# Performance work log

Measured on AMD Instinct MI355X. Metric: run time of the kernel, lower is better.

## Reference

```python
import itertools
import jax, jax.numpy as jnp
import numpy as np

B = 1024      # graphs
N = 40        # atoms per graph (module supports 1..49)
ETA = 64
K = 32        # num_clusters
ZD = 32       # z_dim
NA = 10       # num_atom_types
NB = 5        # num_bond_types + 1
CH, AH, BH = 128, 128, 64
TAU = 1.0


def _resblock(x, W1, b1, W2, b2, Ws, bs):
    # assumed ResidualBlock: Linear->ReLU->(dropout, eval=identity)->Linear + linear skip
    h = jax.nn.relu(x @ W1 + b1)
    return h @ W2 + b2 + (x @ Ws + bs)


def setup_inputs() -> dict:
    key = jax.random.key(0)
    ks = jax.random.split(key, 24)
    s = 0.05
    pairs = np.array(list(itertools.combinations(range(N), 2)), dtype=np.int32)  # [780,2]
    offsets = (np.arange(B, dtype=np.int32) * N)[:, None, None]
    edge_index = jnp.asarray((pairs[None] + offsets).reshape(-1, 2))  # [B*780, 2]
    return {
        "eta": jax.random.normal(ks[0], (B, ETA), jnp.float32),
        "gumbel_noise": jax.random.gumbel(ks[1], (B * N, K), jnp.float32),
        "z_noise": jax.random.normal(ks[2], (B * N, ZD), jnp.float32),
        "cW1": jax.random.normal(ks[3], (ETA, CH)) * s, "cb1": jnp.zeros((CH,)),
        "cW2": jax.random.normal(ks[4], (CH, K)) * s, "cb2": jnp.zeros((K,)),
        "cWs": jax.random.normal(ks[5], (ETA, K)) * s, "cbs": jnp.zeros((K,)),
        "cluster_means": jax.random.normal(ks[6], (K, ZD)),
        "cluster_log_sigmas": jnp.full((K, ZD), -2.0),
        "aW1": jax.random.normal(ks[7], (ZD, AH)) * s, "ab1": jnp.zeros((AH,)),
        "aW2": jax.random.normal(ks[8], (AH, NA)) * s, "ab2": jnp.zeros((NA,)),
        "aWs": jax.random.normal(ks[9], (ZD, NA)) * s, "abs_": jnp.zeros((NA,)),
        "bond_matrix": jax.random.normal(ks[10], (NB, ZD, ZD)),
        "bW1": jax.random.normal(ks[11], (NB, BH)) * s, "bb1": jnp.zeros((BH,)),
        "bW2": jax.random.normal(ks[12], (BH, NB)) * s, "bb2": jnp.zeros((NB,)),
        "bWs": jax.random.normal(ks[13], (NB, NB)) * s, "bbs": jnp.zeros((NB,)),
        "edge_index": edge_index,
    }


def reference(eta, gumbel_noise, z_noise,
              cW1, cb1, cW2, cb2, cWs, cbs,
              cluster_means, cluster_log_sigmas,
              aW1, ab1, aW2, ab2, aWs, abs_,
              bond_matrix, bW1, bb1, bW2, bb2, bWs, bbs,
              edge_index):
    # decode_eta: mixture weights
    pi = jax.nn.softmax(_resblock(eta, cW1, cb1, cW2, cb2, cWs, cbs), axis=1)  # [B,K]
    log_pi = jnp.log(pi)
    # sample_c: gumbel-softmax (hard, straight-through) per node
    logits = jnp.repeat(log_pi, N, axis=0)                      # [B*N, K]
    y_soft = jax.nn.softmax((logits + gumbel_noise) / TAU, axis=-1)
    y_hard = jax.nn.one_hot(jnp.argmax(y_soft, axis=-1), K, dtype=y_soft.dtype)
    c = y_hard + y_soft - jax.lax.stop_gradient(y_soft)         # straight-through
    # sample_z
    mu = c @ cluster_means                                      # [B*N, ZD]
    log_sigma = c @ cluster_log_sigmas
    sigma = jnp.exp(jnp.clip(log_sigma, -20.0, 30.0))
    z = z_noise * sigma + mu
    # decode_z: atom logits
    atom_types = _resblock(z, aW1, ab1, aW2, ab2, aWs, abs_)    # [B*N, NA]
    # symmetrized per-bond-type bilinear form over edge node pairs
    Wsym = 0.5 * (bond_matrix + jnp.swapaxes(bond_matrix, 1, 2))  # [NB, ZD, ZD]
    zi = z[edge_index[:, 0]]                                    # [E, ZD]
    zj = z[edge_index[:, 1]]                                    # [E, ZD]
    bil = jnp.einsum('ed,tdc,ec->et', zi, Wsym, zj)             # [E, NB]
    edge_logits = _resblock(bil, bW1, bb1, bW2, bb2, bWs, bbs)
    edge_types = jax.nn.softmax(edge_logits, axis=1)            # [E, NB]
    return atom_types, edge_types
```

## Files before the change

kernel.cpp:

```cpp
#include <hip/hip_runtime.h>

constexpr int NPAIR = 780;

constexpr int OFF_ZT = 0;
constexpr int OFF_A  = 1280;
constexpr int UTP    = 1280;
constexpr int OFF_BT = 3840;
constexpr int SH_TOT = 7740;

typedef float v2f __attribute__((ext_vector_type(2)));
typedef float v4f __attribute__((ext_vector_type(4)));
union V4 { v4f v; v2f h[2]; float f[4]; };

__device__ __forceinline__ void pk_fma_lo(v2f& acc, v2f s2, v2f b) {
  asm("v_pk_fma_f32 %0, %1, %2, %0 op_sel:[0,0,0] op_sel_hi:[0,1,1]"
      : "+v"(acc) : "v"(s2), "v"(b));
}
__device__ __forceinline__ void pk_fma_hi(v2f& acc, v2f s2, v2f b) {
  asm("v_pk_fma_f32 %0, %1, %2, %0 op_sel:[1,0,0] op_sel_hi:[1,1,1]"
      : "+v"(acc) : "v"(s2), "v"(b));
}
__device__ __forceinline__ void pk_fma_vs(v2f& acc, v2f a, v2f b) {
  asm("v_pk_fma_f32 %0, %1, %2, %0 op_sel:[0,0,0] op_sel_hi:[1,1,1]"
      : "+v"(acc) : "v"(a), "s"(b));
}
__device__ __forceinline__ v2f pk_add(v2f a, v2f b) {
  v2f d; asm("v_pk_add_f32 %0, %1, %2" : "=v"(d) : "v"(a), "v"(b)); return d;
}
__device__ __forceinline__ v2f pk_addrelu(v2f a, v2f b) {
  v2f s = pk_add(a, b);
  v2f d; d.x = fmaxf(s.x, 0.f); d.y = fmaxf(s.y, 0.f);
  return d;
}

__global__ __launch_bounds__(256) void prep_kernel(
    const float* __restrict__ eta,
    const float* __restrict__ cW1, const float* __restrict__ cb1,
    const float* __restrict__ cW2, const float* __restrict__ cb2,
    const float* __restrict__ cWs, const float* __restrict__ cbs,
    const float* __restrict__ bond, const float* __restrict__ lsig,
    const float* __restrict__ bW1, const float* __restrict__ bb1,
    const float* __restrict__ bW2, const float* __restrict__ bb2,
    const float* __restrict__ bWs, const float* __restrict__ bbs,
    float* __restrict__ log_pi, float* __restrict__ wsym,
    float* __restrict__ sigma, float* __restrict__ hwg)
{
  if (blockIdx.x < 256) {
    const int lane = threadIdx.x & 63, wid = threadIdx.x >> 6;
    const int row = blockIdx.x * 4 + wid;
    __shared__ __align__(16) float etas[4][64];
    __shared__ __align__(16) float hs[4][128];
    etas[wid][lane] = eta[row * 64 + lane];
    __syncthreads();
    float a0 = cb1[lane], a1 = cb1[lane + 64];
    for (int d = 0; d < 64; ++d) {
      float ed = etas[wid][d];
      a0 += ed * cW1[d * 128 + lane];
      a1 += ed * cW1[d * 128 + lane + 64];
    }
    hs[wid][lane] = fmaxf(a0, 0.f);
    hs[wid][lane + 64] = fmaxf(a1, 0.f);
    __syncthreads();
    if (lane < 32) {
      float x = cb2[lane] + cbs[lane];
      for (int j = 0; j < 128; ++j) x += hs[wid][j] * cW2[j * 32 + lane];
      for (int d = 0; d < 64; ++d) x += etas[wid][d] * cWs[d * 32 + lane];
      float m = x;
      for (int off = 16; off; off >>= 1) m = fmaxf(m, __shfl_xor(m, off));
      float e = __expf(x - m);
      float s = e;
      for (int off = 16; off; off >>= 1) s += __shfl_xor(s, off);
      log_pi[row * 32 + lane] = (x - m) - __logf(s);
    }
  } else {
    const int e = (blockIdx.x - 256) * 256 + threadIdx.x;
    if (e < 5120) {
      const int t = e >> 10, r = e & 1023, c = r >> 5, d = r & 31;
      wsym[e] = 0.5f * (bond[e] + bond[t * 1024 + d * 32 + c]);
    } else if (e < 6144) {
      const int q = e - 5120;
      sigma[q] = __expf(fminf(fmaxf(lsig[q], -20.f), 30.f));
    } else if (e < 6888) {
      const int idx = e - 6144;
      float v;
      if (idx < 320) v = bW1[idx];
      else if (idx < 384) v = bb1[idx - 320];
      else if (idx < 704) { int qq = idx - 384; int t2 = qq >> 6, j = qq & 63; v = bW2[j * 5 + t2]; }
      else if (idx < 709) v = bb2[idx - 704];
      else if (idx < 734) v = bWs[idx - 709];
      else v = bbs[idx - 734];
      hwg[idx] = v;
    }
  }
}

__global__ __launch_bounds__(256, 5) void fused_kernel(
    const float* __restrict__ log_pi, const float* __restrict__ gumbel,
    const float* __restrict__ z_noise,
    const float* __restrict__ means, const float* __restrict__ sigma,
    const float* __restrict__ aW1, const float* __restrict__ ab1,
    const float* __restrict__ aW2, const float* __restrict__ ab2,
    const float* __restrict__ aWs, const float* __restrict__ abs_,
    const float* __restrict__ wsym, const float* __restrict__ hwg,
    float* __restrict__ atom_out, float* __restrict__ edge_out)
{
  __shared__ __align__(16) float S[SH_TOT];
  const int tid = threadIdx.x;
  const int lane = tid & 63, wid = tid >> 6;
  const int m = blockIdx.x;

  if (lane < 40) {
    const int n = wid * 10 + (lane >> 2);
    const int sub = lane & 3;
    const int c0 = sub * 8;
    const int n_glb = m * 40 + n;
    const float4* lp4 = (const float4*)(log_pi + m * 32 + c0);
    const float4* g4  = (const float4*)(gumbel + (size_t)n_glb * 32 + c0);
    const float4* zn4 = (const float4*)(z_noise + (size_t)n_glb * 32 + c0);
    float4 zn0 = zn4[0], zn1 = zn4[1];
    float vals[8];
    {
      float4 a = lp4[0], b = g4[0];
      vals[0] = a.x + b.x; vals[1] = a.y + b.y; vals[2] = a.z + b.z; vals[3] = a.w + b.w;
    }
    {
      float4 a = lp4[1], b = g4[1];
      vals[4] = a.x + b.x; vals[5] = a.y + b.y; vals[6] = a.z + b.z; vals[7] = a.w + b.w;
    }
    int kb = c0; float vb = vals[0];
    #pragma unroll
    for (int q = 1; q < 8; ++q)
      if (vals[q] > vb) { vb = vals[q]; kb = c0 + q; }
    #pragma unroll
    for (int off = 1; off <= 2; off <<= 1) {
      float vo = __shfl_xor(vb, off);
      int   ko = __shfl_xor(kb, off);
      if (vo > vb || (vo == vb && ko < kb)) { vb = vo; kb = ko; }
    }
    const float4* mk4 = (const float4*)(means + kb * 32 + c0);
    const float4* sg4 = (const float4*)(sigma + kb * 32 + c0);
    {
      float4 mk = mk4[0], sg = sg4[0];
      S[OFF_ZT + (c0    ) * 40 + n] = zn0.x * sg.x + mk.x;
      S[OFF_ZT + (c0 + 1) * 40 + n] = zn0.y * sg.y + mk.y;
      S[OFF_ZT + (c0 + 2) * 40 + n] = zn0.z * sg.z + mk.z;
      S[OFF_ZT + (c0 + 3) * 40 + n] = zn0.w * sg.w + mk.w;
    }
    {
      float4 mk = mk4[1], sg = sg4[1];
      S[OFF_ZT + (c0 + 4) * 40 + n] = zn1.x * sg.x + mk.x;
      S[OFF_ZT + (c0 + 5) * 40 + n] = zn1.y * sg.y + mk.y;
      S[OFF_ZT + (c0 + 6) * 40 + n] = zn1.z * sg.z + mk.z;
      S[OFF_ZT + (c0 + 7) * 40 + n] = zn1.w * sg.w + mk.w;
    }
  }
  __syncthreads();

  {
    for (int u = tid; u < 320; u += 256) {
      const int ng = u >> 5, jg = u & 31;
      const int n0 = ng * 4, j0 = jg * 4;
      v2f acc[4][2];
      #pragma unroll
      for (int a = 0; a < 4; ++a) { acc[a][0] = (v2f){0.f,0.f}; acc[a][1] = (v2f){0.f,0.f}; }
      #pragma unroll 8
      for (int c = 0; c < 32; ++c) {
        V4 zv; zv.v = *(const v4f*)&S[OFF_ZT + c * 40 + n0];
        V4 wv; wv.v = *(const v4f*)(aW1 + c * 128 + j0);
        pk_fma_lo(acc[0][0], zv.h[0], wv.h[0]); pk_fma_lo(acc[0][1], zv.h[0], wv.h[1]);
        pk_fma_hi(acc[1][0], zv.h[0], wv.h[0]); pk_fma_hi(acc[1][1], zv.h[0], wv.h[1]);
        pk_fma_lo(acc[2][0], zv.h[1], wv.h[0]); pk_fma_lo(acc[2][1], zv.h[1], wv.h[1]);
        pk_fma_hi(acc[3][0], zv.h[1], wv.h[0]); pk_fma_hi(acc[3][1], zv.h[1], wv.h[1]);
      }
      V4 bv; bv.v = *(const v4f*)(ab1 + j0);
      #pragma unroll
      for (int a = 0; a < 4; ++a) {
        V4 hv;
        hv.h[0] = pk_addrelu(acc[a][0], bv.h[0]);
        hv.h[1] = pk_addrelu(acc[a][1], bv.h[1]);
        *(v4f*)&S[OFF_A + (n0 + a) * 132 + j0] = hv.v;
      }
    }
  }
  __syncthreads();

  if (tid < 200) {
    const int n = tid / 5, kp = tid - (tid / 5) * 5, k0 = kp * 2;
    float a0 = ab2[k0] + abs_[k0];
    float a1 = ab2[k0 + 1] + abs_[k0 + 1];
    #pragma unroll 8
    for (int c = 0; c < 32; ++c) {
      float zc = S[OFF_ZT + c * 40 + n];
      float2 w = *(const float2*)(aWs + c * 10 + k0);
      a0 += zc * w.x; a1 += zc * w.y;
    }
    #pragma unroll 8
    for (int j = 0; j < 128; ++j) {
      float hv = S[OFF_A + n * 132 + j];
      float2 w = *(const float2*)(aW2 + j * 10 + k0);
      a0 += hv * w.x; a1 += hv * w.y;
    }
    *(float2*)(atom_out + (size_t)m * 400 + n * 10 + k0) = make_float2(a0, a1);
  }
  __syncthreads();

  #pragma unroll
  for (int R = 0; R < 3; ++R) {
    const int tbase = 2 * R;
    const int nplanes = (R == 2) ? 1 : 2;
    if (tid < nplanes * 80) {
      const int tl = tid / 80, r = tid - tl * 80;
      const int dg = r / 10, ig = r - dg * 10;
      const int d0 = dg * 4, i0 = ig * 4;
      const float* wg = wsym + (tbase + tl) * 1024;
      v2f acc[4][2];
      #pragma unroll
      for (int a = 0; a < 4; ++a) { acc[a][0] = (v2f){0.f,0.f}; acc[a][1] = (v2f){0.f,0.f}; }
      #pragma unroll 8
      for (int c = 0; c < 32; ++c) {
        V4 zv; zv.v = *(const v4f*)&S[OFF_ZT + c * 40 + i0];
        V4 wv; wv.v = *(const v4f*)(wg + c * 32 + d0);
        pk_fma_lo(acc[0][0], wv.h[0], zv.h[0]); pk_fma_lo(acc[0][1], wv.h[0], zv.h[1]);
        pk_fma_hi(acc[1][0], wv.h[0], zv.h[0]); pk_fma_hi(acc[1][1], wv.h[0], zv.h[1]);
        pk_fma_lo(acc[2][0], wv.h[1], zv.h[0]); pk_fma_lo(acc[2][1], wv.h[1], zv.h[1]);
        pk_fma_hi(acc[3][0], wv.h[1], zv.h[0]); pk_fma_hi(acc[3][1], wv.h[1], zv.h[1]);
      }
      #pragma unroll
      for (int a = 0; a < 4; ++a) {
        V4 st; st.h[0] = acc[a][0]; st.h[1] = acc[a][1];
        *(v4f*)&S[OFF_A + tl * UTP + (d0 + a) * 40 + i0] = st.v;
      }
    }
    __syncthreads();

    if (tid < nplanes * 55) {
      const int tl = tid / 55;
      int q = tid - tl * 55;
      int ig = 0;
      while (q >= 10 - ig) { q -= 10 - ig; ++ig; }
      const int jg = ig + q;
      const int i0 = ig * 4, j0 = jg * 4;
      v2f acc[4][2];
      #pragma unroll
      for (int a = 0; a < 4; ++a) { acc[a][0] = (v2f){0.f,0.f}; acc[a][1] = (v2f){0.f,0.f}; }
      #pragma unroll 8
      for (int d = 0; d < 32; ++d) {
        V4 uv; uv.v = *(const v4f*)&S[OFF_A + tl * UTP + d * 40 + i0];
        V4 zv; zv.v = *(const v4f*)&S[OFF_ZT + d * 40 + j0];
        pk_fma_lo(acc[0][0], uv.h[0], zv.h[0]); pk_fma_lo(acc[0][1], uv.h[0], zv.h[1]);
        pk_fma_hi(acc[1][0], uv.h[0], zv.h[0]); pk_fma_hi(acc[1][1], uv.h[0], zv.h[1]);
        pk_fma_lo(acc[2][0], uv.h[1], zv.h[0]); pk_fma_lo(acc[2][1], uv.h[1], zv.h[1]);
        pk_fma_hi(acc[3][0], uv.h[1], zv.h[0]); pk_fma_hi(acc[3][1], uv.h[1], zv.h[1]);
      }
      const int tg = tbase + tl;
      #pragma unroll
      for (int a = 0; a < 4; ++a) {
        const int i = i0 + a;
        V4 row; row.h[0] = acc[a][0]; row.h[1] = acc[a][1];
        #pragma unroll
        for (int b = 0; b < 4; ++b) {
          const int j = j0 + b;
          if (i < j) {
            const int p = i * (79 - i) / 2 + (j - i - 1);
            S[OFF_BT + tg * 780 + p] = row.f[b];
          }
        }
      }
    }
    __syncthreads();
  }

  const float* w1h = hwg;
  const float* b1h = hwg + 320;
  const float* w2t = hwg + 384;
  const float* b2h = hwg + 704;
  const float* wsh = hwg + 709;
  const float* bsh = hwg + 734;

  const bool htail = (tid < 12);
  float bil5[3][5];
  v2f bil2[3][5];
  v2f lg2[3][5];
  #pragma unroll
  for (int s = 0; s < 3; ++s) {
    const int p = tid + (s << 8);
    #pragma unroll
    for (int t = 0; t < 5; ++t) {
      float v = S[OFF_BT + t * 780 + p];
      bil5[s][t] = v;
      bil2[s][t].x = v; bil2[s][t].y = v;
    }
    #pragma unroll
    for (int t2 = 0; t2 < 5; ++t2) {
      float a = b2h[t2] + bsh[t2];
      #pragma unroll
      for (int t = 0; t < 5; ++t) a += bil5[s][t] * wsh[t * 5 + t2];
      lg2[s][t2].x = a; lg2[s][t2].y = 0.f;
    }
  }
  float bil3[5], lg3[5];
  if (htail) {
    const int p = 768 + tid;
    #pragma unroll
    for (int t = 0; t < 5; ++t) bil3[t] = S[OFF_BT + t * 780 + p];
    #pragma unroll
    for (int t2 = 0; t2 < 5; ++t2) {
      float a = b2h[t2] + bsh[t2];
      #pragma unroll
      for (int t = 0; t < 5; ++t) a += bil3[t] * wsh[t * 5 + t2];
      lg3[t2] = a;
    }
  }
  {
    for (int j4 = 0; j4 < 16; ++j4) {
      V4 bb; bb.v = *(const v4f*)(b1h + 4 * j4);
      v2f h2[3][2];
      #pragma unroll
      for (int s = 0; s < 3; ++s) { h2[s][0] = bb.h[0]; h2[s][1] = bb.h[1]; }
      #pragma unroll
      for (int t = 0; t < 5; ++t) {
        V4 w1; w1.v = *(const v4f*)(w1h + t * 64 + 4 * j4);
        #pragma unroll
        for (int s = 0; s < 3; ++s) {
          pk_fma_vs(h2[s][0], bil2[s][t], w1.h[0]);
          pk_fma_vs(h2[s][1], bil2[s][t], w1.h[1]);
        }
      }
      #pragma unroll
      for (int s = 0; s < 3; ++s) {
        h2[s][0].x = fmaxf(h2[s][0].x, 0.f); h2[s][0].y = fmaxf(h2[s][0].y, 0.f);
        h2[s][1].x = fmaxf(h2[s][1].x, 0.f); h2[s][1].y = fmaxf(h2[s][1].y, 0.f);
      }
      #pragma unroll
      for (int t2 = 0; t2 < 5; ++t2) {
        V4 w2; w2.v = *(const v4f*)(w2t + t2 * 64 + 4 * j4);
        #pragma unroll
        for (int s = 0; s < 3; ++s) {
          pk_fma_vs(lg2[s][t2], h2[s][0], w2.h[0]);
          pk_fma_vs(lg2[s][t2], h2[s][1], w2.h[1]);
        }
      }
      if (htail) {
        float4 h3 = make_float4(bb.f[0], bb.f[1], bb.f[2], bb.f[3]);
        #pragma unroll
        for (int t = 0; t < 5; ++t) {
          const float* w1p = w1h + t * 64 + 4 * j4;
          float bt = bil3[t];
          h3.x += bt * w1p[0]; h3.y += bt * w1p[1]; h3.z += bt * w1p[2]; h3.w += bt * w1p[3];
        }
        h3.x = fmaxf(h3.x, 0.f); h3.y = fmaxf(h3.y, 0.f);
        h3.z = fmaxf(h3.z, 0.f); h3.w = fmaxf(h3.w, 0.f);
        #pragma unroll
        for (int t2 = 0; t2 < 5; ++t2) {
          const float* w2p = w2t + t2 * 64 + 4 * j4;
          lg3[t2] += h3.x * w2p[0] + h3.y * w2p[1] + h3.z * w2p[2] + h3.w * w2p[3];
        }
      }
    }
  }
  #pragma unroll
  for (int s = 0; s < 3; ++s) {
    const int p = tid + (s << 8);
    float lgv[5];
    #pragma unroll
    for (int t2 = 0; t2 < 5; ++t2) lgv[t2] = lg2[s][t2].x + lg2[s][t2].y;
    float mx = lgv[0];
    #pragma unroll
    for (int t2 = 1; t2 < 5; ++t2) mx = fmaxf(mx, lgv[t2]);
    float e[5], sum = 0.f;
    #pragma unroll
    for (int t2 = 0; t2 < 5; ++t2) { e[t2] = __expf(lgv[t2] - mx); sum += e[t2]; }
    float inv = 1.f / sum;
    float* outp = edge_out + ((size_t)m * NPAIR + p) * 5;
    #pragma unroll
    for (int t2 = 0; t2 < 5; ++t2) outp[t2] = e[t2] * inv;
  }
  if (htail) {
    const int p = 768 + tid;
    float mx = lg3[0];
    #pragma unroll
    for (int t2 = 1; t2 < 5; ++t2) mx = fmaxf(mx, lg3[t2]);
    float e[5], sum = 0.f;
    #pragma unroll
    for (int t2 = 0; t2 < 5; ++t2) { e[t2] = __expf(lg3[t2] - mx); sum += e[t2]; }
    float inv = 1.f / sum;
    float* outp = edge_out + ((size_t)m * NPAIR + p) * 5;
    #pragma unroll
    for (int t2 = 0; t2 < 5; ++t2) outp[t2] = e[t2] * inv;
  }
}

extern "C" void kernel_launch(void* const* d_in, const int* in_sizes, int n_in,
                              void* d_out, int out_size, void* d_ws, size_t ws_size,
                              hipStream_t stream) {
  const float* eta    = (const float*)d_in[0];
  const float* gumbel = (const float*)d_in[1];
  const float* z_noise= (const float*)d_in[2];
  const float* cW1 = (const float*)d_in[3];
  const float* cb1 = (const float*)d_in[4];
  const float* cW2 = (const float*)d_in[5];
  const float* cb2 = (const float*)d_in[6];
  const float* cWs = (const float*)d_in[7];
  const float* cbs = (const float*)d_in[8];
  const float* means = (const float*)d_in[9];
  const float* lsig  = (const float*)d_in[10];
  const float* aW1 = (const float*)d_in[11];
  const float* ab1 = (const float*)d_in[12];
  const float* aW2 = (const float*)d_in[13];
  const float* ab2 = (const float*)d_in[14];
  const float* aWs = (const float*)d_in[15];
  const float* abs_= (const float*)d_in[16];
  const float* bond= (const float*)d_in[17];
  const float* bW1 = (const float*)d_in[18];
  const float* bb1 = (const float*)d_in[19];
  const float* bW2 = (const float*)d_in[20];
  const float* bb2 = (const float*)d_in[21];
  const float* bWs = (const float*)d_in[22];
  const float* bbs = (const float*)d_in[23];

  float* wsym   = (float*)d_ws;
  float* sigma  = wsym + 5120;
  float* hwg    = sigma + 1024;
  float* log_pi = hwg + 768;
  float* atom_out = (float*)d_out;
  float* edge_out = atom_out + (size_t)1024 * 400;

  prep_kernel<<<284, 256, 0, stream>>>(eta, cW1, cb1, cW2, cb2, cWs, cbs,
                                       bond, lsig, bW1, bb1, bW2, bb2, bWs, bbs,
                                       log_pi, wsym, sigma, hwg);
  fused_kernel<<<1024, 256, 0, stream>>>(log_pi, gumbel, z_noise,
                                         means, sigma, aW1, ab1, aW2, ab2, aWs, abs_,
                                         wsym, hwg, atom_out, edge_out);
}
```

Baseline: 182.3 us.

## Pack bilinear scalars, vectorize atom head, merge bond-plane rounds

The atom output head now accumulates two reduction steps at a time with packed FMAs instead of scalar FMAs. The per-edge bilinear values are stored as packed pairs selected through op_sel rather than duplicated into both halves, which cuts register use in the edge MLP. The bond-plane projection runs three planes in the first round and two in the second, so it needs two rounds and barriers instead of three. This needs a larger shared-memory staging area, and the occupancy hint drops from 5 to 4 blocks per CU.

```diff
diff --git a/kernel.cpp b/kernel.cpp
--- a/kernel.cpp
+++ b/kernel.cpp
@@ -5,8 +5,8 @@
 constexpr int OFF_ZT = 0;
 constexpr int OFF_A  = 1280;
 constexpr int UTP    = 1280;
-constexpr int OFF_BT = 3840;
-constexpr int SH_TOT = 7740;
+constexpr int OFF_BT = 5120;
+constexpr int SH_TOT = 9020;
 
 typedef float v2f __attribute__((ext_vector_type(2)));
 typedef float v4f __attribute__((ext_vector_type(4)));
@@ -19,6 +19,14 @@
 __device__ __forceinline__ void pk_fma_hi(v2f& acc, v2f s2, v2f b) {
   asm("v_pk_fma_f32 %0, %1, %2, %0 op_sel:[1,0,0] op_sel_hi:[1,1,1]"
       : "+v"(acc) : "v"(s2), "v"(b));
+}
+__device__ __forceinline__ void pk_fma_lo_s(v2f& acc, v2f s2, v2f b) {
+  asm("v_pk_fma_f32 %0, %1, %2, %0 op_sel:[0,0,0] op_sel_hi:[0,1,1]"
+      : "+v"(acc) : "v"(s2), "s"(b));
+}
+__device__ __forceinline__ void pk_fma_hi_s(v2f& acc, v2f s2, v2f b) {
+  asm("v_pk_fma_f32 %0, %1, %2, %0 op_sel:[1,0,0] op_sel_hi:[1,1,1]"
+      : "+v"(acc) : "v"(s2), "s"(b));
 }
 __device__ __forceinline__ void pk_fma_vs(v2f& acc, v2f a, v2f b) {
   asm("v_pk_fma_f32 %0, %1, %2, %0 op_sel:[0,0,0] op_sel_hi:[1,1,1]"
@@ -94,7 +102,7 @@
   }
 }
 
-__global__ __launch_bounds__(256, 5) void fused_kernel(
+__global__ __launch_bounds__(256, 4) void fused_kernel(
     const float* __restrict__ log_pi, const float* __restrict__ gumbel,
     const float* __restrict__ z_noise,
     const float* __restrict__ means, const float* __restrict__ sigma,
@@ -186,28 +194,35 @@
 
   if (tid < 200) {
     const int n = tid / 5, kp = tid - (tid / 5) * 5, k0 = kp * 2;
-    float a0 = ab2[k0] + abs_[k0];
-    float a1 = ab2[k0 + 1] + abs_[k0 + 1];
+    v2f a01;
+    a01.x = ab2[k0] + abs_[k0];
+    a01.y = ab2[k0 + 1] + abs_[k0 + 1];
     #pragma unroll 8
-    for (int c = 0; c < 32; ++c) {
-      float zc = S[OFF_ZT + c * 40 + n];
-      float2 w = *(const float2*)(aWs + c * 10 + k0);
-      a0 += zc * w.x; a1 += zc * w.y;
+    for (int c = 0; c < 32; c += 2) {
+      v2f zz;
+      zz.x = S[OFF_ZT + c * 40 + n];
+      zz.y = S[OFF_ZT + (c + 1) * 40 + n];
+      v2f w0 = *(const v2f*)(aWs + c * 10 + k0);
+      v2f w1 = *(const v2f*)(aWs + (c + 1) * 10 + k0);
+      pk_fma_lo(a01, zz, w0);
+      pk_fma_hi(a01, zz, w1);
     }
     #pragma unroll 8
-    for (int j = 0; j < 128; ++j) {
-      float hv = S[OFF_A + n * 132 + j];
-      float2 w = *(const float2*)(aW2 + j * 10 + k0);
-      a0 += hv * w.x; a1 += hv * w.y;
-    }
-    *(float2*)(atom_out + (size_t)m * 400 + n * 10 + k0) = make_float2(a0, a1);
+    for (int j = 0; j < 128; j += 2) {
+      v2f hh = *(const v2f*)&S[OFF_A + n * 132 + j];
+      v2f w0 = *(const v2f*)(aW2 + j * 10 + k0);
+      v2f w1 = *(const v2f*)(aW2 + (j + 1) * 10 + k0);
+      pk_fma_lo(a01, hh, w0);
+      pk_fma_hi(a01, hh, w1);
+    }
+    *(float2*)(atom_out + (size_t)m * 400 + n * 10 + k0) = make_float2(a01.x, a01.y);
   }
   __syncthreads();
 
   #pragma unroll
-  for (int R = 0; R < 3; ++R) {
-    const int tbase = 2 * R;
-    const int nplanes = (R == 2) ? 1 : 2;
+  for (int R = 0; R < 2; ++R) {
+    const int tbase = (R == 0) ? 0 : 3;
+    const int nplanes = (R == 0) ? 3 : 2;
     if (tid < nplanes * 80) {
       const int tl = tid / 80, r = tid - tl * 80;
       const int dg = r / 10, ig = r - dg * 10;
@@ -278,23 +293,25 @@
   const float* bsh = hwg + 734;
 
   const bool htail = (tid < 12);
-  float bil5[3][5];
-  v2f bil2[3][5];
+  v2f bilp[3][3];
   v2f lg2[3][5];
   #pragma unroll
   for (int s = 0; s < 3; ++s) {
     const int p = tid + (s << 8);
-    #pragma unroll
-    for (int t = 0; t < 5; ++t) {
-      float v = S[OFF_BT + t * 780 + p];
-      bil5[s][t] = v;
-      bil2[s][t].x = v; bil2[s][t].y = v;
-    }
+    bilp[s][0].x = S[OFF_BT + 0 * 780 + p];
+    bilp[s][0].y = S[OFF_BT + 1 * 780 + p];
+    bilp[s][1].x = S[OFF_BT + 2 * 780 + p];
+    bilp[s][1].y = S[OFF_BT + 3 * 780 + p];
+    bilp[s][2].x = S[OFF_BT + 4 * 780 + p];
+    bilp[s][2].y = 0.f;
     #pragma unroll
     for (int t2 = 0; t2 < 5; ++t2) {
       float a = b2h[t2] + bsh[t2];
-      #pragma unroll
-      for (int t = 0; t < 5; ++t) a += bil5[s][t] * wsh[t * 5 + t2];
+      a += bilp[s][0].x * wsh[0 * 5 + t2];
+      a += bilp[s][0].y * wsh[1 * 5 + t2];
+      a += bilp[s][1].x * wsh[2 * 5 + t2];
+      a += bilp[s][1].y * wsh[3 * 5 + t2];
+      a += bilp[s][2].x * wsh[4 * 5 + t2];
       lg2[s][t2].x = a; lg2[s][t2].y = 0.f;
     }
   }
@@ -322,8 +339,13 @@
         V4 w1; w1.v = *(const v4f*)(w1h + t * 64 + 4 * j4);
         #pragma unroll
         for (int s = 0; s < 3; ++s) {
-          pk_fma_vs(h2[s][0], bil2[s][t], w1.h[0]);
-          pk_fma_vs(h2[s][1], bil2[s][t], w1.h[1]);
+          if (t & 1) {
+            pk_fma_hi_s(h2[s][0], bilp[s][t >> 1], w1.h[0]);
+            pk_fma_hi_s(h2[s][1], bilp[s][t >> 1], w1.h[1]);
+          } else {
+            pk_fma_lo_s(h2[s][0], bilp[s][t >> 1], w1.h[0]);
+            pk_fma_lo_s(h2[s][1], bilp[s][t >> 1], w1.h[1]);
+          }
         }
       }
       #pragma unroll
```

New measurement: 173.9 us. 4.6% less time.
